# Kernel tuning notes

Measured on AMD Instinct MI355X. Metric: run time of the kernel, lower is better.

The kernel has to match this reference:

```python
import jax, jax.numpy as jnp
import numpy as np

N, F, E, A, H = 50000, 64, 1600000, 8, 16
RECEPTIVE_FIELD = 7


def setup_inputs() -> dict:
    key = jax.random.key(0)
    ks = jax.random.split(key, 12)
    inp = {
        "x": jax.random.normal(ks[0], (N, F), dtype=jnp.float32),
        "edge_index": jax.random.randint(ks[1], (2, E), 0, N, dtype=jnp.int64),
        "w1": jax.random.normal(ks[2], (F, H), dtype=jnp.float32) * 0.1,
        "b1": jax.random.normal(ks[3], (H,), dtype=jnp.float32) * 0.1,
        "w2": jax.random.normal(ks[4], (H, H), dtype=jnp.float32) * 0.1,
        "b2": jax.random.normal(ks[5], (H,), dtype=jnp.float32) * 0.1,
        "w3": jax.random.normal(ks[6], (H, F), dtype=jnp.float32) * 0.1,
        "b3": jax.random.normal(ks[7], (F,), dtype=jnp.float32) * 0.1,
        "fc1_w": jax.random.normal(ks[8], ((1 + RECEPTIVE_FIELD) * F, F), dtype=jnp.float32) * 0.05,
        "fc1_b": jax.random.normal(ks[9], (F,), dtype=jnp.float32) * 0.05,
        "fc2_w": jax.random.normal(ks[10], (F, A), dtype=jnp.float32) * 0.1,
        "fc2_b": jax.random.normal(ks[11], (A,), dtype=jnp.float32) * 0.1,
    }
    return inp


def _mlp(x, w1, b1, w2, b2, w3, b3):
    h = jax.nn.relu(x @ w1 + b1)
    h = jax.nn.relu(h @ w2 + b2)
    return h @ w3 + b3


def _agg_mean(x, src, dst):
    # scatter-mean: mean of source-node features over incoming edges per target
    s = jax.ops.segment_sum(x[src], dst, num_segments=N)          # [N, F]
    cnt = jax.ops.segment_sum(jnp.ones((src.shape[0], 1), x.dtype), dst, num_segments=N)
    return s / jnp.maximum(cnt, 1.0)  # nodes with no in-edges -> 0 (torch mean aggr)


def reference(x, edge_index, w1, b1, w2, b2, w3, b3, fc1_w, fc1_b, fc2_w, fc2_b):
    src, dst = edge_index[0], edge_index[1]
    mlp = lambda t: _mlp(t, w1, b1, w2, b2, w3, b3)
    fields = [mlp(mlp(x))]
    for i in range(RECEPTIVE_FIELD):
        x_ = mlp(x)
        for _ in range(i + 1):
            x_ = _agg_mean(x_, src, dst)
        fields.append(mlp(x_))
    f = jnp.concatenate(fields, axis=1)          # [N, 8*F]
    h = f @ fc1_w + fc1_b                        # [N, F]
    logits = h @ fc2_w + fc2_b                   # [N, A]
    return jax.nn.softmax(logits, axis=-1)       # Categorical probs
```

## Files before the change

### kernel.cpp

```cpp
#include <hip/hip_runtime.h>


#define NB2MAX 400
#define NBLK   256
#define CAP2   32
#define CAPC   48
#define CAPB   6144
#define OVCAP  1024
#define LCAP   6144
#define CAPN   64

__global__ __launch_bounds__(1024) void binfill_k(
    const int* __restrict__ src, const int* __restrict__ dst, int E, int n,
    int* __restrict__ gcur, int* __restrict__ ovbuf,
    int* __restrict__ bins, int* __restrict__ cnts,
    const float* __restrict__ w1, const float* __restrict__ w3,
    const float* __restrict__ b3, const float* __restrict__ fc1w,
    const float* __restrict__ fc1b, const float* __restrict__ fc2w,
    const float* __restrict__ fc2b,
    float* __restrict__ M, float* __restrict__ cvec,
    float* __restrict__ W31, float* __restrict__ c31) {
    __shared__ int lbuf[NB2MAX * CAP2];
    __shared__ int lcnt[NB2MAX];
    __shared__ int lflush[NB2MAX];
    int tid = threadIdx.x;
    int NB = (n + 127) >> 7;

    if ((int)blockIdx.x >= NBLK) {
        float* fl = (float*)lbuf;
        int s = (int)blockIdx.x - NBLK;
        if (s == 0) {
            if (tid < 256) {
                int i = tid >> 4, j = tid & 15;
                float a = 0.f;
                for (int g = 0; g < 64; g++) a += w3[i * 64 + g] * w1[g * 16 + j];
                W31[tid] = a;
            } else if (tid < 272) {
                int j = tid - 256;
                float a = 0.f;
                for (int g = 0; g < 64; g++) a += b3[g] * w1[g * 16 + j];
                c31[j] = a;
            } else if (tid >= 320 && tid < 384) {
                int h = tid - 320;
                float a = 0.f;
                for (int r = 0; r < 512; r++) a += b3[r & 63] * fc1w[r * 64 + h];
                fl[h] = a;
            }
            __syncthreads();
            if (tid < 8) {
                float a = fc2b[tid];
                for (int h = 0; h < 64; h++) a += (fc1b[h] + fl[h]) * fc2w[h * 8 + tid];
                cvec[tid] = a;
            }
        } else {
            int k = s - 1;
            {
                int i = tid >> 6, h = tid & 63;
                float a = 0.f;
                const float* f1 = fc1w + (size_t)(k * 64) * 64 + h;
                for (int g = 0; g < 64; g++) a += w3[i * 64 + g] * f1[g * 64];
                fl[i * 64 + h] = a;
            }
            __syncthreads();
            if (tid < 128) {
                int i = tid >> 3, j = tid & 7;
                float a = 0.f;
                for (int h = 0; h < 64; h++) a += fl[i * 64 + h] * fc2w[h * 8 + j];
                M[k * 128 + i * 8 + j] = a;
            }
        }
        return;
    }

    for (int b = tid; b < NB; b += 1024) { lcnt[b] = 0; lflush[b] = 0; }
    __syncthreads();
    int blk = blockIdx.x;
    int chunk = (E + NBLK - 1) / NBLK;
    int beg = blk * chunk;
    int end = beg + chunk; if (end > E) end = E;
    for (int t0 = beg; t0 < end; t0 += 1024) {
        int e = t0 + tid;
        if (e < end) {
            int d = dst[e], s = src[e];
            if ((unsigned)d < (unsigned)n && (unsigned)s < (unsigned)n) {
                int b = d >> 7;
                int pk = ((d & 127) << 16) | s;
                int pos = atomicAdd(&lcnt[b], 1);
                if (pos < CAP2) lbuf[b * CAP2 + pos] = pk;
                else {
                    int p = atomicAdd(&gcur[b], 1);
                    if (p < OVCAP) ovbuf[b * OVCAP + p] = pk;
                }
            }
        }
        __syncthreads();
        for (int b = tid; b < NB; b += 1024) {
            int cnt = lcnt[b]; if (cnt > CAP2) cnt = CAP2;
            int fl2 = lflush[b];
            size_t cell = ((size_t)b * NBLK + blk) * CAPC;
            int base = 0;
            while (cnt - base >= 16) {
                if (fl2 + 16 <= CAPC) {
                    int* dp = bins + cell + fl2;
                    #pragma unroll
                    for (int q = 0; q < 16; q++) dp[q] = lbuf[b * CAP2 + base + q];
                    fl2 += 16;
                } else {
                    int p = atomicAdd(&gcur[b], 16);
                    for (int q = 0; q < 16; q++)
                        if (p + q < OVCAP) ovbuf[b * OVCAP + p + q] = lbuf[b * CAP2 + base + q];
                }
                base += 16;
            }
            int rem = cnt - base;
            if (base > 0)
                for (int q = 0; q < rem; q++) lbuf[b * CAP2 + q] = lbuf[b * CAP2 + base + q];
            lcnt[b] = rem; lflush[b] = fl2;
        }
        __syncthreads();
    }
    for (int b = tid; b < NB; b += 1024) {
        int cnt = lcnt[b]; if (cnt > CAP2) cnt = CAP2;
        int fl2 = lflush[b];
        size_t cell = ((size_t)b * NBLK + blk) * CAPC;
        if (fl2 + cnt <= CAPC) {
            for (int q = 0; q < cnt; q++) bins[cell + fl2 + q] = lbuf[b * CAP2 + q];
            fl2 += cnt;
        } else {
            int p = atomicAdd(&gcur[b], cnt);
            for (int q = 0; q < cnt; q++)
                if (p + q < OVCAP) ovbuf[b * OVCAP + p + q] = lbuf[b * CAP2 + q];
        }
        cnts[(size_t)blk * NB + b] = fl2;
    }
}

__global__ __launch_bounds__(256) void csr2_k(
    const int* __restrict__ bins, const int* __restrict__ cnts,
    const int* __restrict__ gcur, const int* __restrict__ ovbuf,
    unsigned short* __restrict__ csrp, int* __restrict__ degs,
    int* __restrict__ csr, int2* __restrict__ be, int n) {
    __shared__ int hist[128], pref[128], cur[128];
    __shared__ int scnt[NBLK];
    __shared__ int lbuf[LCAP];
    __shared__ int sov;
    int tid = threadIdx.x;
    int NB = (n + 127) >> 7;
    int b = blockIdx.x;
    if (tid < 128) { hist[tid] = 0; cur[tid] = 0; }
    scnt[tid] = cnts[(size_t)tid * NB + b];
    if (tid == 0) {
        int g = gcur[b];
        sov = g < 0 ? 0 : (g > OVCAP ? OVCAP : g);
    }
    __syncthreads();
    {
        int c = scnt[tid];
        size_t cell = ((size_t)b * NBLK + tid) * CAPC;
        for (int i = 0; i < c; i++) atomicAdd(&hist[bins[cell + i] >> 16], 1);
    }
    if (tid == 0)
        for (int i = 0; i < sov; i++) atomicAdd(&hist[ovbuf[b * OVCAP + i] >> 16], 1);
    __syncthreads();
    if (tid == 0) {
        int r = 0;
        for (int i = 0; i < 128; i++) { pref[i] = r; r += hist[i]; }
    }
    __syncthreads();
    {
        int c = scnt[tid];
        size_t cell = ((size_t)b * NBLK + tid) * CAPC;
        for (int i = 0; i < c; i++) {
            int pk = bins[cell + i];
            int dl = pk >> 16;
            int pos = pref[dl] + atomicAdd(&cur[dl], 1);
            if (pos < LCAP) lbuf[pos] = pk & 0xffff;
        }
    }
    if (tid == 0) {
        for (int i = 0; i < sov; i++) {
            int pk = ovbuf[b * OVCAP + i];
            int dl = pk >> 16;
            int pos = pref[dl] + atomicAdd(&cur[dl], 1);
            if (pos < LCAP) lbuf[pos] = pk & 0xffff;
        }
    }
    __syncthreads();
    for (int q = tid; q < 128 * CAPN; q += 256) {
        int dl = q >> 6, j = q & 63;
        int d = (b << 7) + dl;
        if (d >= n) break;
        int cnt = hist[dl];
        int v = (j < cnt) ? lbuf[pref[dl] + j] : n;
        int pos = ((j & 3) << 4) | (j >> 2);
        csrp[(size_t)d * CAPN + pos] = (unsigned short)v;
    }
    if (tid < 128) {
        int d = (b << 7) + tid;
        if (d < n) {
            int cnt = hist[tid];
            degs[d] = cnt;
            if (cnt > CAPN) {
                int s0 = b * CAPB + pref[tid];
                be[d] = make_int2(s0 + CAPN, s0 + cnt);
                for (int j = CAPN; j < cnt; j++)
                    csr[s0 + j] = lbuf[pref[tid] + j] << 2;
            }
        }
    }
}

__global__ __launch_bounds__(256) void proj_k(
    const float* __restrict__ x, float* __restrict__ z0, float* __restrict__ z1,
    float* __restrict__ logits,
    const float* __restrict__ w1, const float* __restrict__ b1,
    const float* __restrict__ w2, const float* __restrict__ b2,
    const float* __restrict__ W31, const float* __restrict__ c31,
    const float* __restrict__ M0, const float* __restrict__ cvec, int n) {
    __shared__ float sw1[1024], sw2[256], sW[256], sM[128];
    __shared__ float sb1[16], sb2[16], sc[16], scv[8];
    int tid = threadIdx.x;
    for (int i = tid; i < 1024; i += 256) sw1[i] = w1[i];
    sw2[tid] = w2[tid & 255];
    sW[tid & 255] = W31[tid & 255];
    if (tid < 128) sM[tid] = M0[tid];
    if (tid < 16) { sb1[tid] = b1[tid]; sb2[tid] = b2[tid]; sc[tid] = c31[tid]; }
    if (tid < 8) scv[tid] = cvec[tid];
    __syncthreads();
    if (blockIdx.x == 0 && tid < 16) {
        z0[(size_t)n * 16 + tid] = 0.f;
        z1[(size_t)n * 16 + tid] = 0.f;
    }
    int nid = blockIdx.x * 256 + tid;
    if (nid >= n) return;
    float t1[16];
    #pragma unroll
    for (int j = 0; j < 16; j++) t1[j] = sb1[j];
    const float4* xp = (const float4*)(x + (size_t)nid * 64);
    #pragma unroll
    for (int q = 0; q < 16; q++) {
        float4 v = xp[q];
        #pragma unroll
        for (int j = 0; j < 16; j++)
            t1[j] += v.x * sw1[(4 * q) * 16 + j] + v.y * sw1[(4 * q + 1) * 16 + j]
                   + v.z * sw1[(4 * q + 2) * 16 + j] + v.w * sw1[(4 * q + 3) * 16 + j];
    }
    #pragma unroll
    for (int j = 0; j < 16; j++) t1[j] = fmaxf(t1[j], 0.f);
    float t2[16];
    #pragma unroll
    for (int j = 0; j < 16; j++) {
        float a = sb2[j];
        #pragma unroll
        for (int i = 0; i < 16; i++) a += t1[i] * sw2[i * 16 + j];
        t2[j] = fmaxf(a, 0.f);
    }
    float z[16];
    #pragma unroll
    for (int j = 0; j < 16; j++) {
        float a = sc[j];
        #pragma unroll
        for (int i = 0; i < 16; i++) a += t2[i] * sW[i * 16 + j];
        z[j] = a;
    }
    float4* zo = (float4*)(z0 + (size_t)nid * 16);
    #pragma unroll
    for (int q = 0; q < 4; q++)
        zo[q] = make_float4(z[4 * q], z[4 * q + 1], z[4 * q + 2], z[4 * q + 3]);
    float h[16], f2[16];
    #pragma unroll
    for (int i = 0; i < 16; i++) h[i] = fmaxf(z[i] + sb1[i], 0.f);
    #pragma unroll
    for (int j = 0; j < 16; j++) {
        float a = sb2[j];
        #pragma unroll
        for (int i = 0; i < 16; i++) a += h[i] * sw2[i * 16 + j];
        f2[j] = fmaxf(a, 0.f);
    }
    float* lp = logits + (size_t)nid * 8;
    #pragma unroll
    for (int j = 0; j < 8; j++) {
        float l = scv[j];
        #pragma unroll
        for (int i = 0; i < 16; i++) l += f2[i] * sM[i * 8 + j];
        lp[j] = l;
    }
}

__global__ __launch_bounds__(256, 4) void hop_k(
    const float* __restrict__ zin, float* __restrict__ zout, float* __restrict__ logits,
    const unsigned short* __restrict__ csrp, const int* __restrict__ degs,
    const int2* __restrict__ be, const int* __restrict__ csr,
    const float* __restrict__ w2, const float* __restrict__ b1,
    const float* __restrict__ b2, const float* __restrict__ M, int n, int FB) {
    __shared__ float sw2[256], sM[128], sb1[16], sb2[16];
    int tid = threadIdx.x;
    if ((int)blockIdx.x < FB) {
        sw2[tid] = w2[tid];
        if (tid < 128) sM[tid] = M[tid];
        if (tid < 16) { sb1[tid] = b1[tid]; sb2[tid] = b2[tid]; }
        __syncthreads();
        int nid = blockIdx.x * 256 + tid;
        if (nid >= n) return;
        float h[16];
        const float4* zp = (const float4*)(zin + (size_t)nid * 16);
        #pragma unroll
        for (int q = 0; q < 4; q++) {
            float4 v = zp[q];
            h[4 * q] = v.x; h[4 * q + 1] = v.y; h[4 * q + 2] = v.z; h[4 * q + 3] = v.w;
        }
        #pragma unroll
        for (int i = 0; i < 16; i++) h[i] = fmaxf(h[i] + sb1[i], 0.f);
        float t2[16];
        #pragma unroll
        for (int j = 0; j < 16; j++) {
            float a = sb2[j];
            #pragma unroll
            for (int i = 0; i < 16; i++) a += h[i] * sw2[i * 16 + j];
            t2[j] = fmaxf(a, 0.f);
        }
        float* lp = logits + (size_t)nid * 8;
        #pragma unroll
        for (int j = 0; j < 8; j++) {
            float l = 0.f;
            #pragma unroll
            for (int i = 0; i < 16; i++) l += t2[i] * sM[i * 8 + j];
            lp[j] += l;
        }
        return;
    }
    int wave = tid >> 6;
    int lane = tid & 63;
    int quarter = lane >> 4;
    int l16 = lane & 15;
    int t = l16 >> 2, c = l16 & 3;
    int node = (((int)blockIdx.x - FB) * 4 + wave) * 4 + quarter;
    if (node >= n) return;
    int degi = degs[node];
    const uint4* ip = (const uint4*)(csrp + ((size_t)node << 6));
    uint4 pa = ip[t * 2];
    uint4 pb = ip[t * 2 + 1];
    int r0 = pa.x & 0xffff, r1 = pa.x >> 16;
    int r2 = pa.y & 0xffff, r3 = pa.y >> 16;
    int r4 = pa.z & 0xffff, r5 = pa.z >> 16;
    int r6 = pa.w & 0xffff, r7 = pa.w >> 16;
    int r8 = pb.x & 0xffff, r9 = pb.x >> 16;
    int rA = pb.y & 0xffff, rB = pb.y >> 16;
    int rC = pb.z & 0xffff, rD = pb.z >> 16;
    int rE = pb.w & 0xffff, rF = pb.w >> 16;
    const float4* z4 = (const float4*)zin;
    float4 v0 = z4[((size_t)r0 << 2) + c];
    float4 v1 = z4[((size_t)r1 << 2) + c];
    float4 v2 = z4[((size_t)r2 << 2) + c];
    float4 v3 = z4[((size_t)r3 << 2) + c];
    float4 v4 = z4[((size_t)r4 << 2) + c];
    float4 v5 = z4[((size_t)r5 << 2) + c];
    float4 v6 = z4[((size_t)r6 << 2) + c];
    float4 v7 = z4[((size_t)r7 << 2) + c];
    float4 v8 = z4[((size_t)r8 << 2) + c];
    float4 v9 = z4[((size_t)r9 << 2) + c];
    float4 vA = z4[((size_t)rA << 2) + c];
    float4 vB = z4[((size_t)rB << 2) + c];
    float4 vC = z4[((size_t)rC << 2) + c];
    float4 vD = z4[((size_t)rD << 2) + c];
    float4 vE = z4[((size_t)rE << 2) + c];
    float4 vF = z4[((size_t)rF << 2) + c];
    float ax = (((v0.x + v1.x) + (v2.x + v3.x)) + ((v4.x + v5.x) + (v6.x + v7.x)))
             + (((v8.x + v9.x) + (vA.x + vB.x)) + ((vC.x + vD.x) + (vE.x + vF.x)));
    float ay = (((v0.y + v1.y) + (v2.y + v3.y)) + ((v4.y + v5.y) + (v6.y + v7.y)))
             + (((v8.y + v9.y) + (vA.y + vB.y)) + ((vC.y + vD.y) + (vE.y + vF.y)));
    float az = (((v0.z + v1.z) + (v2.z + v3.z)) + ((v4.z + v5.z) + (v6.z + v7.z)))
             + (((v8.z + v9.z) + (vA.z + vB.z)) + ((vC.z + vD.z) + (vE.z + vF.z)));
    float aw = (((v0.w + v1.w) + (v2.w + v3.w)) + ((v4.w + v5.w) + (v6.w + v7.w)))
             + (((v8.w + v9.w) + (vA.w + vB.w)) + ((vC.w + vD.w) + (vE.w + vF.w)));
    if (degi > CAPN) {
        int2 r = be[node];
        for (int q = r.x + t; q < r.y; q += 4) {
            float4 v = z4[(size_t)csr[q] + c];
            ax += v.x; ay += v.y; az += v.z; aw += v.w;
        }
    }
    #pragma unroll
    for (int off = 8; off >= 4; off >>= 1) {
        ax += __shfl_down(ax, off, 16);
        ay += __shfl_down(ay, off, 16);
        az += __shfl_down(az, off, 16);
        aw += __shfl_down(aw, off, 16);
    }
    if (l16 < 4) {
        float inv = 1.f / (float)(degi > 0 ? degi : 1);
        ((float4*)(zout + (size_t)node * 16))[l16] =
            make_float4(ax * inv, ay * inv, az * inv, aw * inv);
    }
}

__global__ __launch_bounds__(256) void fieldsoft_k(
    const float* __restrict__ z, float* __restrict__ logits,
    const float* __restrict__ w2, const float* __restrict__ b1,
    const float* __restrict__ b2, const float* __restrict__ M, int n) {
    __shared__ float sw2[256], sM[128], sb1[16], sb2[16];
    int tid = threadIdx.x;
    sw2[tid] = w2[tid];
    if (tid < 128) sM[tid] = M[tid];
    if (tid < 16) { sb1[tid] = b1[tid]; sb2[tid] = b2[tid]; }
    __syncthreads();
    int nid = blockIdx.x * 256 + tid;
    if (nid >= n) return;
    float h[16];
    const float4* zp = (const float4*)(z + (size_t)nid * 16);
    #pragma unroll
    for (int q = 0; q < 4; q++) {
        float4 v = zp[q];
        h[4 * q] = v.x; h[4 * q + 1] = v.y; h[4 * q + 2] = v.z; h[4 * q + 3] = v.w;
    }
    #pragma unroll
    for (int i = 0; i < 16; i++) h[i] = fmaxf(h[i] + sb1[i], 0.f);
    float t2[16];
    #pragma unroll
    for (int j = 0; j < 16; j++) {
        float a = sb2[j];
        #pragma unroll
        for (int i = 0; i < 16; i++) a += h[i] * sw2[i * 16 + j];
        t2[j] = fmaxf(a, 0.f);
    }
    float4* lp4 = (float4*)(logits + (size_t)nid * 8);
    float4 l0 = lp4[0], l1 = lp4[1];
    float v[8] = {l0.x, l0.y, l0.z, l0.w, l1.x, l1.y, l1.z, l1.w};
    #pragma unroll
    for (int j = 0; j < 8; j++) {
        float l = 0.f;
        #pragma unroll
        for (int i = 0; i < 16; i++) l += t2[i] * sM[i * 8 + j];
        v[j] += l;
    }
    float m = v[0];
    #pragma unroll
    for (int j = 1; j < 8; j++) m = fmaxf(m, v[j]);
    float s = 0.f;
    #pragma unroll
    for (int j = 0; j < 8; j++) { v[j] = expf(v[j] - m); s += v[j]; }
    float inv = 1.f / s;
    lp4[0] = make_float4(v[0] * inv, v[1] * inv, v[2] * inv, v[3] * inv);
    lp4[1] = make_float4(v[4] * inv, v[5] * inv, v[6] * inv, v[7] * inv);
}

extern "C" void kernel_launch(void* const* d_in, const int* in_sizes, int n_in,
                              void* d_out, int out_size, void* d_ws, size_t ws_size,
                              hipStream_t stream) {
    const float* x    = (const float*)d_in[0];
    const int*   ei   = (const int*)d_in[1];
    const float* w1   = (const float*)d_in[2];
    const float* b1   = (const float*)d_in[3];
    const float* w2   = (const float*)d_in[4];
    const float* b2   = (const float*)d_in[5];
    const float* w3   = (const float*)d_in[6];
    const float* b3   = (const float*)d_in[7];
    const float* fc1w = (const float*)d_in[8];
    const float* fc1b = (const float*)d_in[9];
    const float* fc2w = (const float*)d_in[10];
    const float* fc2b = (const float*)d_in[11];
    float* out = (float*)d_out;

    int n = in_sizes[0] / 64;
    int E = in_sizes[1] / 2;
    int NB = (n + 127) >> 7;
    const int* src = ei;
    const int* dst = ei + E;

    char* ws = (char*)d_ws;
    auto carve = [&](size_t bytes) {
        char* p = ws;
        ws += (bytes + 255) & ~((size_t)255);
        return p;
    };
    int*   gcur    = (int*)carve((size_t)NB * 4);
    int*   ovbuf   = (int*)carve((size_t)NB * OVCAP * 4);
    int*   binsbuf = (int*)carve((size_t)NB * NBLK * CAPC * 4);
    int*   cnts    = (int*)carve((size_t)NBLK * NB * 4);
    unsigned short* csrp = (unsigned short*)carve((size_t)n * CAPN * 2);
    int*   degs    = (int*)carve((size_t)n * 4);
    int*   csr     = (int*)carve((size_t)NB * CAPB * 4);
    int2*  be      = (int2*)carve((size_t)n * 8);
    float* buf0    = (float*)carve((size_t)(n + 1) * 16 * 4);
    float* buf1    = (float*)carve((size_t)(n + 1) * 16 * 4);
    float* M       = (float*)carve(1024 * 4);
    float* cvec    = (float*)carve(8 * 4);
    float* W31     = (float*)carve(256 * 4);
    float* c31     = (float*)carve(16 * 4);

    hipMemsetAsync(gcur, 0, (size_t)NB * 4, stream);
    binfill_k<<<NBLK + 9, 1024, 0, stream>>>(src, dst, E, n, gcur, ovbuf, binsbuf, cnts,
                                             w1, w3, b3, fc1w, fc1b, fc2w, fc2b,
                                             M, cvec, W31, c31);

    int FB = (n + 255) / 256;
    int AB = (n + 15) / 16;
    csr2_k<<<NB, 256, 0, stream>>>(binsbuf, cnts, gcur, ovbuf, csrp, degs, csr, be, n);
    proj_k<<<FB, 256, 0, stream>>>(x, buf0, buf1, out, w1, b1, w2, b2,
                                   W31, c31, M, cvec, n);

    float* cur = buf0;
    float* nxt = buf1;
    hop_k<<<AB, 256, 0, stream>>>(cur, nxt, out, csrp, degs, be, csr,
                                  w2, b1, b2, M, n, 0);
    { float* t = cur; cur = nxt; nxt = t; }
    for (int k = 1; k <= 6; k++) {
        hop_k<<<FB + AB, 256, 0, stream>>>(cur, nxt, out, csrp, degs, be, csr,
                                           w2, b1, b2, M + k * 128, n, FB);
        float* t = cur; cur = nxt; nxt = t;
    }
    fieldsoft_k<<<FB, 256, 0, stream>>>(cur, out, w2, b1, b2, M + 7 * 128, n);
}
```

Baseline: 255.9 us.

## Bucket nodes by degree tier to skip padded neighbor gathers

Result: no change. 255.2 us (-0.3%).

```diff
diff --git a/kernel.cpp b/kernel.cpp
--- a/kernel.cpp
+++ b/kernel.cpp
@@ -139,15 +139,18 @@
     const int* __restrict__ bins, const int* __restrict__ cnts,
     const int* __restrict__ gcur, const int* __restrict__ ovbuf,
     unsigned short* __restrict__ csrp, int* __restrict__ degs,
-    int* __restrict__ csr, int2* __restrict__ be, int n) {
+    int* __restrict__ csr, int2* __restrict__ be,
+    int* __restrict__ lists, int* __restrict__ lcnt3, int n) {
     __shared__ int hist[128], pref[128], cur[128];
     __shared__ int scnt[NBLK];
     __shared__ int lbuf[LCAP];
     __shared__ int sov;
+    __shared__ int ccnt[3], cbase[3];
     int tid = threadIdx.x;
     int NB = (n + 127) >> 7;
     int b = blockIdx.x;
     if (tid < 128) { hist[tid] = 0; cur[tid] = 0; }
+    if (tid < 3) ccnt[tid] = 0;
     scnt[tid] = cnts[(size_t)tid * NB + b];
     if (tid == 0) {
         int g = gcur[b];
@@ -195,11 +198,14 @@
         int pos = ((j & 3) << 4) | (j >> 2);
         csrp[(size_t)d * CAPN + pos] = (unsigned short)v;
     }
+    int myc = -1, lpos = 0;
     if (tid < 128) {
         int d = (b << 7) + tid;
         if (d < n) {
             int cnt = hist[tid];
             degs[d] = cnt;
+            myc = cnt <= 32 ? 0 : (cnt <= 48 ? 1 : 2);
+            lpos = atomicAdd(&ccnt[myc], 1);
             if (cnt > CAPN) {
                 int s0 = b * CAPB + pref[tid];
                 be[d] = make_int2(s0 + CAPN, s0 + cnt);
@@ -208,6 +214,10 @@
             }
         }
     }
+    __syncthreads();
+    if (tid < 3) cbase[tid] = atomicAdd(&lcnt3[tid], ccnt[tid]);
+    __syncthreads();
+    if (myc >= 0) lists[(size_t)myc * n + cbase[myc] + lpos] = (b << 7) + tid;
 }
 
 __global__ __launch_bounds__(256) void proj_k(
@@ -291,6 +301,7 @@
     const float* __restrict__ zin, float* __restrict__ zout, float* __restrict__ logits,
     const unsigned short* __restrict__ csrp, const int* __restrict__ degs,
     const int2* __restrict__ be, const int* __restrict__ csr,
+    const int* __restrict__ lists, const int* __restrict__ lcnt3,
     const float* __restrict__ w2, const float* __restrict__ b1,
     const float* __restrict__ b2, const float* __restrict__ M, int n, int FB) {
     __shared__ float sw2[256], sM[128], sb1[16], sb2[16];
@@ -334,20 +345,21 @@
     int quarter = lane >> 4;
     int l16 = lane & 15;
     int t = l16 >> 2, c = l16 & 3;
-    int node = (((int)blockIdx.x - FB) * 4 + wave) * 4 + quarter;
-    if (node >= n) return;
+    int idx = (((int)blockIdx.x - FB) * 4 + wave) * 4 + quarter;
+    if (idx >= n) return;
+    int ns = lcnt3[0];
+    int nm = lcnt3[1];
+    int tier, node;
+    if (idx < ns)           { tier = 0; node = lists[idx]; }
+    else if (idx < ns + nm) { tier = 1; node = lists[(size_t)n + (idx - ns)]; }
+    else                    { tier = 2; node = lists[2 * (size_t)n + (idx - ns - nm)]; }
     int degi = degs[node];
     const uint4* ip = (const uint4*)(csrp + ((size_t)node << 6));
     uint4 pa = ip[t * 2];
-    uint4 pb = ip[t * 2 + 1];
     int r0 = pa.x & 0xffff, r1 = pa.x >> 16;
     int r2 = pa.y & 0xffff, r3 = pa.y >> 16;
     int r4 = pa.z & 0xffff, r5 = pa.z >> 16;
     int r6 = pa.w & 0xffff, r7 = pa.w >> 16;
-    int r8 = pb.x & 0xffff, r9 = pb.x >> 16;
-    int rA = pb.y & 0xffff, rB = pb.y >> 16;
-    int rC = pb.z & 0xffff, rD = pb.z >> 16;
-    int rE = pb.w & 0xffff, rF = pb.w >> 16;
     const float4* z4 = (const float4*)zin;
     float4 v0 = z4[((size_t)r0 << 2) + c];
     float4 v1 = z4[((size_t)r1 << 2) + c];
@@ -357,27 +369,40 @@
     float4 v5 = z4[((size_t)r5 << 2) + c];
     float4 v6 = z4[((size_t)r6 << 2) + c];
     float4 v7 = z4[((size_t)r7 << 2) + c];
-    float4 v8 = z4[((size_t)r8 << 2) + c];
-    float4 v9 = z4[((size_t)r9 << 2) + c];
-    float4 vA = z4[((size_t)rA << 2) + c];
-    float4 vB = z4[((size_t)rB << 2) + c];
-    float4 vC = z4[((size_t)rC << 2) + c];
-    float4 vD = z4[((size_t)rD << 2) + c];
-    float4 vE = z4[((size_t)rE << 2) + c];
-    float4 vF = z4[((size_t)rF << 2) + c];
-    float ax = (((v0.x + v1.x) + (v2.x + v3.x)) + ((v4.x + v5.x) + (v6.x + v7.x)))
-             + (((v8.x + v9.x) + (vA.x + vB.x)) + ((vC.x + vD.x) + (vE.x + vF.x)));
-    float ay = (((v0.y + v1.y) + (v2.y + v3.y)) + ((v4.y + v5.y) + (v6.y + v7.y)))
-             + (((v8.y + v9.y) + (vA.y + vB.y)) + ((vC.y + vD.y) + (vE.y + vF.y)));
-    float az = (((v0.z + v1.z) + (v2.z + v3.z)) + ((v4.z + v5.z) + (v6.z + v7.z)))
-             + (((v8.z + v9.z) + (vA.z + vB.z)) + ((vC.z + vD.z) + (vE.z + vF.z)));
-    float aw = (((v0.w + v1.w) + (v2.w + v3.w)) + ((v4.w + v5.w) + (v6.w + v7.w)))
-             + (((v8.w + v9.w) + (vA.w + vB.w)) + ((vC.w + vD.w) + (vE.w + vF.w)));
-    if (degi > CAPN) {
-        int2 r = be[node];
-        for (int q = r.x + t; q < r.y; q += 4) {
-            float4 v = z4[(size_t)csr[q] + c];
-            ax += v.x; ay += v.y; az += v.z; aw += v.w;
+    float ax = ((v0.x + v1.x) + (v2.x + v3.x)) + ((v4.x + v5.x) + (v6.x + v7.x));
+    float ay = ((v0.y + v1.y) + (v2.y + v3.y)) + ((v4.y + v5.y) + (v6.y + v7.y));
+    float az = ((v0.z + v1.z) + (v2.z + v3.z)) + ((v4.z + v5.z) + (v6.z + v7.z));
+    float aw = ((v0.w + v1.w) + (v2.w + v3.w)) + ((v4.w + v5.w) + (v6.w + v7.w));
+    if (tier >= 1) {
+        uint4 pb = ip[t * 2 + 1];
+        int r8 = pb.x & 0xffff, r9 = pb.x >> 16;
+        int rA = pb.y & 0xffff, rB = pb.y >> 16;
+        float4 v8 = z4[((size_t)r8 << 2) + c];
+        float4 v9 = z4[((size_t)r9 << 2) + c];
+        float4 vA = z4[((size_t)rA << 2) + c];
+        float4 vB = z4[((size_t)rB << 2) + c];
+        ax += (v8.x + v9.x) + (vA.x + vB.x);
+        ay += (v8.y + v9.y) + (vA.y + vB.y);
+        az += (v8.z + v9.z) + (vA.z + vB.z);
+        aw += (v8.w + v9.w) + (vA.w + vB.w);
+        if (tier == 2) {
+            int rC = pb.z & 0xffff, rD = pb.z >> 16;
+            int rE = pb.w & 0xffff, rF = pb.w >> 16;
+            float4 vC = z4[((size_t)rC << 2) + c];
+            float4 vD = z4[((size_t)rD << 2) + c];
+            float4 vE = z4[((size_t)rE << 2) + c];
+            float4 vF = z4[((size_t)rF << 2) + c];
+            ax += (vC.x + vD.x) + (vE.x + vF.x);
+            ay += (vC.y + vD.y) + (vE.y + vF.y);
+            az += (vC.z + vD.z) + (vE.z + vF.z);
+            aw += (vC.w + vD.w) + (vE.w + vF.w);
+            if (degi > CAPN) {
+                int2 r = be[node];
+                for (int q = r.x + t; q < r.y; q += 4) {
+                    float4 v = z4[(size_t)csr[q] + c];
+                    ax += v.x; ay += v.y; az += v.z; aw += v.w;
+                }
+            }
         }
     }
     #pragma unroll
@@ -474,6 +499,7 @@
         return p;
     };
     int*   gcur    = (int*)carve((size_t)NB * 4);
+    int*   lcnt3   = (int*)carve(16);
     int*   ovbuf   = (int*)carve((size_t)NB * OVCAP * 4);
     int*   binsbuf = (int*)carve((size_t)NB * NBLK * CAPC * 4);
     int*   cnts    = (int*)carve((size_t)NBLK * NB * 4);
@@ -481,6 +507,7 @@
     int*   degs    = (int*)carve((size_t)n * 4);
     int*   csr     = (int*)carve((size_t)NB * CAPB * 4);
     int2*  be      = (int2*)carve((size_t)n * 8);
+    int*   lists   = (int*)carve((size_t)3 * n * 4);
     float* buf0    = (float*)carve((size_t)(n + 1) * 16 * 4);
     float* buf1    = (float*)carve((size_t)(n + 1) * 16 * 4);
     float* M       = (float*)carve(1024 * 4);
@@ -488,24 +515,27 @@
     float* W31     = (float*)carve(256 * 4);
     float* c31     = (float*)carve(16 * 4);
 
-    hipMemsetAsync(gcur, 0, (size_t)NB * 4, stream);
+    size_t gpad = ((size_t)NB * 4 + 255) & ~((size_t)255);
+    hipMemsetAsync(gcur, 0, gpad + 16, stream);
     binfill_k<<<NBLK + 9, 1024, 0, stream>>>(src, dst, E, n, gcur, ovbuf, binsbuf, cnts,
                                              w1, w3, b3, fc1w, fc1b, fc2w, fc2b,
                                              M, cvec, W31, c31);
 
     int FB = (n + 255) / 256;
     int AB = (n + 15) / 16;
-    csr2_k<<<NB, 256, 0, stream>>>(binsbuf, cnts, gcur, ovbuf, csrp, degs, csr, be, n);
+    csr2_k<<<NB, 256, 0, stream>>>(binsbuf, cnts, gcur, ovbuf, csrp, degs, csr, be,
+                                   lists, lcnt3, n);
     proj_k<<<FB, 256, 0, stream>>>(x, buf0, buf1, out, w1, b1, w2, b2,
                                    W31, c31, M, cvec, n);
 
     float* cur = buf0;
     float* nxt = buf1;
-    hop_k<<<AB, 256, 0, stream>>>(cur, nxt, out, csrp, degs, be, csr,
+    hop_k<<<AB, 256, 0, stream>>>(cur, nxt, out, csrp, degs, be, csr, lists, lcnt3,
                                   w2, b1, b2, M, n, 0);
     { float* t = cur; cur = nxt; nxt = t; }
     for (int k = 1; k <= 6; k++) {
         hop_k<<<FB + AB, 256, 0, stream>>>(cur, nxt, out, csrp, degs, be, csr,
+                                           lists, lcnt3,
                                            w2, b1, b2, M + k * 128, n, FB);
         float* t = cur; cur = nxt; nxt = t;
     }
```
